# Kernel optimization log

Hardware: AMD Instinct MI355X
Metric: run time of the kernel (lower is better)

Reference implementation:

```python
import jax, jax.numpy as jnp
import numpy as np

S, D_IN, D_OUT = 4096, 1024, 1024

def setup_inputs() -> dict:
    key = jax.random.key(0)
    kx, kq, kk, kv = jax.random.split(key, 4)
    scale = 0.02
    return {
        "x": jax.random.normal(kx, (S, D_IN), dtype=jnp.float32),
        "W_query": jax.random.normal(kq, (D_IN, D_OUT), dtype=jnp.float32) * scale,
        "W_key": jax.random.normal(kk, (D_IN, D_OUT), dtype=jnp.float32) * scale,
        "W_value": jax.random.normal(kv, (D_IN, D_OUT), dtype=jnp.float32) * scale,
    }

def reference(x, W_query, W_key, W_value):
    # x: [S, d_in]; W_*: [d_in, d_out]
    queries = x @ W_query        # [S, d_out]
    keys = x @ W_key             # [S, d_out]
    values = x @ W_value         # [S, d_out]
    d_k = keys.shape[-1]
    attn_scores = queries @ keys.T            # [S, S]
    attn_weights = jax.nn.softmax(attn_scores / jnp.sqrt(jnp.float32(d_k)), axis=-1)
    context_vec = attn_weights @ values       # [S, d_out]
    return context_vec
```

## Files before the change

### kernel.cpp

```cpp
#include <hip/hip_runtime.h>

typedef _Float16 f16x8 __attribute__((ext_vector_type(8)));
typedef float f32x4 __attribute__((ext_vector_type(4)));
typedef unsigned short u16;
typedef u16 u16x8 __attribute__((ext_vector_type(8)));
typedef u16 u16x4 __attribute__((ext_vector_type(4)));

__device__ __forceinline__ u16 f2h_bits(float f) {
    _Float16 h = (_Float16)f;
    return __builtin_bit_cast(u16, h);
}
__device__ __forceinline__ float h2f(u16 b) {
    return (float)__builtin_bit_cast(_Float16, b);
}

typedef __attribute__((address_space(1))) unsigned int gu32_as1;
typedef __attribute__((address_space(3))) unsigned int lu32_as3;
__device__ __forceinline__ void gload16(const u16* g, u16* l) {
    __builtin_amdgcn_global_load_lds((gu32_as1*)g, (lu32_as3*)l, 16, 0, 0);
}

#define BAR   __builtin_amdgcn_s_barrier()
#define LGK0  asm volatile("s_waitcnt lgkmcnt(0)" ::: "memory")
#define VM4   asm volatile("s_waitcnt vmcnt(4)" ::: "memory")
#define VM0   asm volatile("s_waitcnt vmcnt(0)" ::: "memory")
#define PRIO1 __builtin_amdgcn_s_setprio(1)
#define PRIO0 __builtin_amdgcn_s_setprio(0)

template <int MODE>
__global__ __launch_bounds__(512, 2) void gemm_bt(
    const u16* __restrict__ A, int lda,
    const u16* __restrict__ B, int ldb,
    u16* __restrict__ C, int ldc,
    int Ksplit, float alpha, size_t c_z_stride,
    int bnW, int bmW, int numPanelX,
    float* __restrict__ rowsum, u16* __restrict__ vt)
{
    __shared__ __attribute__((aligned(16))) u16 As[32768];
    __shared__ __attribute__((aligned(16))) u16 Bs[32768];

    const int t    = threadIdx.x;
    const int lane = t & 63;
    const int wave = t >> 6;
    const int wm   = wave >> 2;
    const int wn   = wave & 3;
    const int l16  = lane & 15;
    const int quad = lane >> 4;

    const int lin = blockIdx.y * gridDim.x + blockIdx.x;
    const int xcd = lin & 7;
    const int idx = lin >> 3;
    const int px  = xcd % numPanelX;
    const int py  = xcd / numPanelX;
    const int bn  = px * bnW + idx % bnW;
    const int bm  = py * bmW + idx / bnW;

    const int kz = blockIdx.z;
    A += (size_t)kz * Ksplit;
    B += (size_t)kz * Ksplit;
    C += (size_t)kz * c_z_stride;

    const int srow = t >> 3;
    const int sseg = ((t & 7) ^ ((t >> 3) & 7)) * 8;
    const u16* Ag = A + (size_t)(bm * 256 + srow) * lda + sseg;
    const u16* Bg = B + (size_t)(bn * 256 + srow) * ldb + sseg;
    u16* AsD = &As[t * 8];
    u16* BsD = &Bs[t * 8];

#define STG_A(h, bufv, kt) do {                                         \
        const u16* _s = Ag + (size_t)(h) * 128 * lda + (size_t)(kt) * 64; \
        u16* _d = AsD + (bufv) * 16384 + (h) * 8192;                    \
        gload16(_s, _d);                                                \
        gload16(_s + (size_t)64 * lda, _d + 4096);                      \
    } while (0)
#define STG_B(h, bufv, kt) do {                                         \
        const u16* _s = Bg + (size_t)(h) * 128 * ldb + (size_t)(kt) * 64; \
        u16* _d = BsD + (bufv) * 16384 + (h) * 8192;                    \
        gload16(_s, _d);                                                \
        gload16(_s + (size_t)64 * ldb, _d + 4096);                      \
    } while (0)

    const int skz = l16 & 7;
    const int sk0 = (quad ^ skz) * 8;
    const int sk1 = ((4 + quad) ^ skz) * 8;
    const u16* Ab = As + wm * 8192 + l16 * 64;
    const u16* Bb = Bs + (wn >> 1) * 8192 + (wn & 1) * 4096 + l16 * 64;

#define RD_A(dst, mh, bufv) do {                                        \
        _Pragma("unroll") for (int mi = 0; mi < 4; mi++) {              \
            dst[mi][0] = *(const f16x8*)(Ab + (bufv) * 16384 +          \
                                         (mh) * 4096 + mi * 1024 + sk0);\
            dst[mi][1] = *(const f16x8*)(Ab + (bufv) * 16384 +          \
                                         (mh) * 4096 + mi * 1024 + sk1);\
        } } while (0)
#define RD_B(dst, nh, bufv) do {                                        \
        _Pragma("unroll") for (int nj = 0; nj < 2; nj++) {              \
            dst[nj][0] = *(const f16x8*)(Bb + (bufv) * 16384 +          \
                                         (nh) * 2048 + nj * 1024 + sk0);\
            dst[nj][1] = *(const f16x8*)(Bb + (bufv) * 16384 +          \
                                         (nh) * 2048 + nj * 1024 + sk1);\
        } } while (0)
#define MFQ(mh, nh, Af, Bf) do {                                        \
        _Pragma("unroll") for (int mi = 0; mi < 4; mi++)                \
        _Pragma("unroll") for (int nj = 0; nj < 2; nj++)                \
        _Pragma("unroll") for (int kk = 0; kk < 2; kk++)                \
            acc[(mh)*4+mi][(nh)*2+nj] =                                 \
                __builtin_amdgcn_mfma_f32_16x16x32_f16(                 \
                    Af[mi][kk], Bf[nj][kk], acc[(mh)*4+mi][(nh)*2+nj],  \
                    0, 0, 0);                                           \
    } while (0)

    f32x4 acc[8][4] = {};
    const int NI = Ksplit >> 7;

    STG_A(0, 0, 0); STG_A(1, 0, 0); STG_B(0, 0, 0); STG_B(1, 0, 0);
    STG_B(0, 1, 1); STG_B(1, 1, 1);
    VM4;
    BAR;

    for (int it = 0; it < NI; ++it) {
        const int t0 = it * 2, t1 = it * 2 + 1;
        const bool nl = (it + 1 < NI);
        f16x8 a0[4][2], a1[4][2], b0[2][2], b1[2][2];

        RD_A(a0, 0, 0); RD_B(b0, 0, 0);
        STG_A(0, 1, t1);
        BAR; LGK0; PRIO1; MFQ(0, 0, a0, b0); PRIO0; BAR;
        RD_B(b1, 1, 0);
        STG_A(1, 1, t1);
        BAR; LGK0; PRIO1; MFQ(0, 1, a0, b1); PRIO0; BAR;
        RD_A(a1, 1, 0);
        if (nl) STG_B(0, 0, t0 + 2);
        BAR; LGK0; PRIO1; MFQ(1, 0, a1, b0); PRIO0; BAR;
        if (nl) STG_B(1, 0, t0 + 2);
        BAR; LGK0; PRIO1; MFQ(1, 1, a1, b1); PRIO0;
        if (nl) VM4; else VM0;
        BAR;
        RD_A(a0, 0, 1); RD_B(b0, 0, 1);
        if (nl) STG_A(0, 0, t0 + 2);
        BAR; LGK0; PRIO1; MFQ(0, 0, a0, b0); PRIO0; BAR;
        RD_B(b1, 1, 1);
        if (nl) STG_A(1, 0, t0 + 2);
        BAR; LGK0; PRIO1; MFQ(0, 1, a0, b1); PRIO0; BAR;
        RD_A(a1, 1, 1);
        if (nl) STG_B(0, 1, t1 + 2);
        BAR; LGK0; PRIO1; MFQ(1, 0, a1, b0); PRIO0; BAR;
        if (nl) STG_B(1, 1, t1 + 2);
        BAR; LGK0; PRIO1; MFQ(1, 1, a1, b1); PRIO0;
        if (nl) VM4; else VM0;
        BAR;
    }
#undef STG_A
#undef STG_B
#undef RD_A
#undef RD_B
#undef MFQ

    const int crow = bm * 256 + wm * 128 + quad * 4;
    const int ccol = bn * 256 + wn * 64 + l16;

    if (MODE == 1) {
        float rs[8][4];
#pragma unroll
        for (int mi = 0; mi < 8; mi++)
#pragma unroll
            for (int r = 0; r < 4; r++) rs[mi][r] = 0.f;
#pragma unroll
        for (int mi = 0; mi < 8; mi++) {
#pragma unroll
            for (int ni = 0; ni < 4; ni++) {
#pragma unroll
                for (int r = 0; r < 4; r++) {
                    float e = __expf(acc[mi][ni][r] * alpha);
                    rs[mi][r] += e;
                    C[(size_t)(crow + mi * 16 + r) * ldc + (ccol + ni * 16)] = f2h_bits(e);
                }
            }
        }
#pragma unroll
        for (int mi = 0; mi < 8; mi++) {
#pragma unroll
            for (int r = 0; r < 4; r++) {
                float s = rs[mi][r];
#pragma unroll
                for (int o = 1; o < 16; o <<= 1) s += __shfl_xor(s, o);
                if (l16 == 0)
                    atomicAdd(&rowsum[crow + mi * 16 + r], s);
            }
        }
    } else if (MODE == 2 && bn >= 8) {
#pragma unroll
        for (int ni = 0; ni < 4; ni++) {
            const int cV = (bn - 8) * 256 + wn * 64 + ni * 16 + l16;
#pragma unroll
            for (int mi = 0; mi < 8; mi++) {
                u16x4 o;
#pragma unroll
                for (int r = 0; r < 4; r++) o[r] = f2h_bits(acc[mi][ni][r]);
                *(u16x4*)(vt + (size_t)cV * 4096 + crow + mi * 16) = o;
            }
        }
    } else {
#pragma unroll
        for (int mi = 0; mi < 8; mi++)
#pragma unroll
            for (int ni = 0; ni < 4; ni++)
#pragma unroll
                for (int r = 0; r < 4; r++)
                    C[(size_t)(crow + mi * 16 + r) * ldc + (ccol + ni * 16)] =
                        f2h_bits(acc[mi][ni][r] * alpha);
    }
}

__global__ __launch_bounds__(256) void cast_to_f16(
    const float* __restrict__ in, u16* __restrict__ out, int n)
{
    int i = (blockIdx.x * 256 + threadIdx.x) * 4;
    if (i + 3 < n) {
        float4 v = *(const float4*)(in + i);
        ushort4 o;
        o.x = f2h_bits(v.x);
        o.y = f2h_bits(v.y);
        o.z = f2h_bits(v.z);
        o.w = f2h_bits(v.w);
        *(ushort4*)(out + i) = o;
    }
}

__global__ __launch_bounds__(256) void transpose_w3(
    const float* __restrict__ W0, const float* __restrict__ W1,
    const float* __restrict__ W2, u16* __restrict__ out)
{
    const float* in = (blockIdx.z == 0) ? W0 : (blockIdx.z == 1) ? W1 : W2;
    u16* o = out + (size_t)blockIdx.z * 1024 * 1024;
    __shared__ float tile[32][33];
    const int bx = blockIdx.x * 32;
    const int by = blockIdx.y * 32;
    const int tx = threadIdx.x, ty = threadIdx.y;
#pragma unroll
    for (int j = 0; j < 4; j++)
        tile[ty + j * 8][tx] = in[(size_t)(by + ty + j * 8) * 1024 + bx + tx];
    __syncthreads();
#pragma unroll
    for (int j = 0; j < 4; j++)
        o[(size_t)(bx + ty + j * 8) * 1024 + by + tx] = f2h_bits(tile[tx][ty + j * 8]);
}

__global__ __launch_bounds__(256) void zero_f32(float* __restrict__ p, int n)
{
    int i = (blockIdx.x * 256 + threadIdx.x) * 4;
    if (i + 3 < n) *(float4*)(p + i) = float4{0.f, 0.f, 0.f, 0.f};
}

__global__ __launch_bounds__(256) void add_div4(
    const u16* __restrict__ P, const float* __restrict__ l,
    float* __restrict__ o)
{
    const size_t zs = (size_t)4096 * 1024;
    int i = (blockIdx.x * 256 + threadIdx.x) * 8;
    float inv = 1.0f / l[i >> 10];
    float s[8] = {};
#pragma unroll
    for (int z = 0; z < 4; z++) {
        u16x8 h = *(const u16x8*)(P + z * zs + i);
#pragma unroll
        for (int j = 0; j < 8; j++) s[j] += h2f(h[j]);
    }
    float4 lo{s[0] * inv, s[1] * inv, s[2] * inv, s[3] * inv};
    float4 hi{s[4] * inv, s[5] * inv, s[6] * inv, s[7] * inv};
    *(float4*)(o + i) = lo;
    *(float4*)(o + i + 4) = hi;
}

extern "C" void kernel_launch(void* const* d_in, const int* in_sizes, int n_in,
                              void* d_out, int out_size, void* d_ws, size_t ws_size,
                              hipStream_t stream)
{
    (void)in_sizes; (void)n_in; (void)out_size; (void)ws_size;
    const float* x  = (const float*)d_in[0];
    const float* Wq = (const float*)d_in[1];
    const float* Wk = (const float*)d_in[2];
    const float* Wv = (const float*)d_in[3];
    float* out = (float*)d_out;
    char* ws = (char*)d_ws;

    u16* xb  = (u16*)(ws);
    u16* Wt  = (u16*)(ws + ((size_t)8  << 20));
    u16* QK  = (u16*)(ws + ((size_t)14 << 20));
    u16* Sb  = (u16*)(ws + ((size_t)32 << 20));
    u16* Vt  = (u16*)(ws + ((size_t)64 << 20));
    float* lr = (float*)(ws + ((size_t)72 << 20));
    u16* P   = (u16*)(ws);

    const int S = 4096, D = 1024;
    dim3 tb(32, 8);

    cast_to_f16<<<(S * D) / (4 * 256), 256, 0, stream>>>(x, xb, S * D);

    transpose_w3<<<dim3(32, 32, 3), tb, 0, stream>>>(Wq, Wk, Wv, Wt);

    gemm_bt<2><<<dim3(12, 16, 1), 512, 0, stream>>>(
        xb, D, Wt, D, QK, 2048, D, 1.0f, 0, 3, 8, 4, nullptr, Vt);

    zero_f32<<<S / (4 * 256), 256, 0, stream>>>(lr, S);

    gemm_bt<1><<<dim3(16, 16, 1), 512, 0, stream>>>(
        QK, 2048, QK + 1024, 2048, Sb, S, D, 0.03125f, 0, 4, 8, 4, lr, nullptr);

    gemm_bt<0><<<dim3(4, 16, 4), 512, 0, stream>>>(
        Sb, S, Vt, S, P, D, 1024, 1.0f, (size_t)S * D, 1, 8, 4, nullptr, nullptr);

    add_div4<<<(S * D) / (8 * 256), 256, 0, stream>>>(P, lr, out);
}
```

Baseline: 216.4 us.

## Deepen GEMM prefetch schedule and merge prep kernels into one launch

The GEMM main loop reorders its global-to-LDS staging so that each half-tile is prefetched earlier, keeping up to six loads in flight (vmcnt 6 instead of 4). This should hide more global latency behind the MFMA work. Separately, the cast, weight transpose and row-sum zeroing kernels are merged into a single launch to cut per-launch overhead. The reordered staging risks LDS buffer hazards if a buffer is overwritten while it is still being read, and the extra in-flight loads raise pressure on the memory system.

Result: faster. 209.7 us, median of 2 (-3.1%).

```diff
diff --git a/kernel.cpp b/kernel.cpp
--- a/kernel.cpp
+++ b/kernel.cpp
@@ -22,7 +22,7 @@
 
 #define BAR   __builtin_amdgcn_s_barrier()
 #define LGK0  asm volatile("s_waitcnt lgkmcnt(0)" ::: "memory")
-#define VM4   asm volatile("s_waitcnt vmcnt(4)" ::: "memory")
+#define VM6   asm volatile("s_waitcnt vmcnt(6)" ::: "memory")
 #define VM0   asm volatile("s_waitcnt vmcnt(0)" ::: "memory")
 #define PRIO1 __builtin_amdgcn_s_setprio(1)
 #define PRIO0 __builtin_amdgcn_s_setprio(0)
@@ -114,8 +114,8 @@
     const int NI = Ksplit >> 7;
 
     STG_A(0, 0, 0); STG_A(1, 0, 0); STG_B(0, 0, 0); STG_B(1, 0, 0);
-    STG_B(0, 1, 1); STG_B(1, 1, 1);
-    VM4;
+    STG_B(0, 1, 1); STG_A(0, 1, 1); STG_B(1, 1, 1);
+    VM6;
     BAR;
 
     for (int it = 0; it < NI; ++it) {
@@ -124,30 +124,30 @@
         f16x8 a0[4][2], a1[4][2], b0[2][2], b1[2][2];
 
         RD_A(a0, 0, 0); RD_B(b0, 0, 0);
-        STG_A(0, 1, t1);
+        STG_A(1, 1, t1);
         BAR; LGK0; PRIO1; MFQ(0, 0, a0, b0); PRIO0; BAR;
         RD_B(b1, 1, 0);
-        STG_A(1, 1, t1);
+        if (nl) STG_B(0, 0, t0 + 2);
         BAR; LGK0; PRIO1; MFQ(0, 1, a0, b1); PRIO0; BAR;
         RD_A(a1, 1, 0);
-        if (nl) STG_B(0, 0, t0 + 2);
+        if (nl) STG_A(0, 0, t0 + 2);
         BAR; LGK0; PRIO1; MFQ(1, 0, a1, b0); PRIO0; BAR;
         if (nl) STG_B(1, 0, t0 + 2);
         BAR; LGK0; PRIO1; MFQ(1, 1, a1, b1); PRIO0;
-        if (nl) VM4; else VM0;
+        if (nl) VM6; else VM0;
         BAR;
         RD_A(a0, 0, 1); RD_B(b0, 0, 1);
-        if (nl) STG_A(0, 0, t0 + 2);
+        if (nl) STG_A(1, 0, t0 + 2);
         BAR; LGK0; PRIO1; MFQ(0, 0, a0, b0); PRIO0; BAR;
         RD_B(b1, 1, 1);
-        if (nl) STG_A(1, 0, t0 + 2);
+        if (nl) STG_B(0, 1, t1 + 2);
         BAR; LGK0; PRIO1; MFQ(0, 1, a0, b1); PRIO0; BAR;
         RD_A(a1, 1, 1);
-        if (nl) STG_B(0, 1, t1 + 2);
+        if (nl) STG_A(0, 1, t1 + 2);
         BAR; LGK0; PRIO1; MFQ(1, 0, a1, b0); PRIO0; BAR;
         if (nl) STG_B(1, 1, t1 + 2);
         BAR; LGK0; PRIO1; MFQ(1, 1, a1, b1); PRIO0;
-        if (nl) VM4; else VM0;
+        if (nl) VM6; else VM0;
         BAR;
     }
 #undef STG_A
@@ -212,44 +212,45 @@
     }
 }
 
-__global__ __launch_bounds__(256) void cast_to_f16(
-    const float* __restrict__ in, u16* __restrict__ out, int n)
+__global__ __launch_bounds__(256) void prep(
+    const float* __restrict__ x, u16* __restrict__ xb,
+    const float* __restrict__ W0, const float* __restrict__ W1,
+    const float* __restrict__ W2, u16* __restrict__ Wt,
+    float* __restrict__ lr)
 {
-    int i = (blockIdx.x * 256 + threadIdx.x) * 4;
-    if (i + 3 < n) {
-        float4 v = *(const float4*)(in + i);
+    __shared__ float tile[32][33];
+    const int bid = blockIdx.x;
+    const int t   = threadIdx.x;
+
+    if (bid < 4096) {
+        int i = (bid * 256 + t) * 4;
+        float4 v = *(const float4*)(x + i);
         ushort4 o;
         o.x = f2h_bits(v.x);
         o.y = f2h_bits(v.y);
         o.z = f2h_bits(v.z);
         o.w = f2h_bits(v.w);
-        *(ushort4*)(out + i) = o;
+        *(ushort4*)(xb + i) = o;
+    } else if (bid < 4096 + 3072) {
+        const int b   = bid - 4096;
+        const int z   = b >> 10;
+        const int rem = b & 1023;
+        const float* in = (z == 0) ? W0 : (z == 1) ? W1 : W2;
+        u16* o = Wt + (size_t)z * 1024 * 1024;
+        const int bx = (rem & 31) * 32;
+        const int by = (rem >> 5) * 32;
+        const int tx = t & 31, ty = t >> 5;
+#pragma unroll
+        for (int j = 0; j < 4; j++)
+            tile[ty + j * 8][tx] = in[(size_t)(by + ty + j * 8) * 1024 + bx + tx];
+        __syncthreads();
+#pragma unroll
+        for (int j = 0; j < 4; j++)
+            o[(size_t)(bx + ty + j * 8) * 1024 + by + tx] = f2h_bits(tile[tx][ty + j * 8]);
+    } else {
+        int i = ((bid - 4096 - 3072) * 256 + t) * 4;
+        *(float4*)(lr + i) = float4{0.f, 0.f, 0.f, 0.f};
     }
-}
-
-__global__ __launch_bounds__(256) void transpose_w3(
-    const float* __restrict__ W0, const float* __restrict__ W1,
-    const float* __restrict__ W2, u16* __restrict__ out)
-{
-    const float* in = (blockIdx.z == 0) ? W0 : (blockIdx.z == 1) ? W1 : W2;
-    u16* o = out + (size_t)blockIdx.z * 1024 * 1024;
-    __shared__ float tile[32][33];
-    const int bx = blockIdx.x * 32;
-    const int by = blockIdx.y * 32;
-    const int tx = threadIdx.x, ty = threadIdx.y;
-#pragma unroll
-    for (int j = 0; j < 4; j++)
-        tile[ty + j * 8][tx] = in[(size_t)(by + ty + j * 8) * 1024 + bx + tx];
-    __syncthreads();
-#pragma unroll
-    for (int j = 0; j < 4; j++)
-        o[(size_t)(bx + ty + j * 8) * 1024 + by + tx] = f2h_bits(tile[tx][ty + j * 8]);
-}
-
-__global__ __launch_bounds__(256) void zero_f32(float* __restrict__ p, int n)
-{
-    int i = (blockIdx.x * 256 + threadIdx.x) * 4;
-    if (i + 3 < n) *(float4*)(p + i) = float4{0.f, 0.f, 0.f, 0.f};
 }
 
 __global__ __launch_bounds__(256) void add_div4(
@@ -293,17 +294,12 @@
     u16* P   = (u16*)(ws);
 
     const int S = 4096, D = 1024;
-    dim3 tb(32, 8);
-
-    cast_to_f16<<<(S * D) / (4 * 256), 256, 0, stream>>>(x, xb, S * D);
-
-    transpose_w3<<<dim3(32, 32, 3), tb, 0, stream>>>(Wq, Wk, Wv, Wt);
+
+    prep<<<4096 + 3072 + 4, 256, 0, stream>>>(x, xb, Wq, Wk, Wv, Wt, lr);
 
     gemm_bt<2><<<dim3(12, 16, 1), 512, 0, stream>>>(
         xb, D, Wt, D, QK, 2048, D, 1.0f, 0, 3, 8, 4, nullptr, Vt);
 
-    zero_f32<<<S / (4 * 256), 256, 0, stream>>>(lr, S);
-
     gemm_bt<1><<<dim3(16, 16, 1), 512, 0, stream>>>(
         QK, 2048, QK + 1024, 2048, Sb, S, D, 0.03125f, 0, 4, 8, 4, lr, nullptr);
 
```
